# Performance work log

Hardware: AMD Instinct MI355X
Metric: run time of the kernel (lower is better)

## Reference

```python
import jax, jax.numpy as jnp
import numpy as np

N = 4096       # number of graph nodes
F_IN = 512     # in_features == out_features (residual connection requires it)
H = 8          # n_heads


def setup_inputs() -> dict:
    key = jax.random.key(0)
    k1, k2, k3, k4, k5 = jax.random.split(key, 5)
    s = 1.0 / np.sqrt(F_IN)  # keep projections well-scaled
    x = jax.random.normal(k1, (N, F_IN), dtype=jnp.float32)
    Wq = jax.random.normal(k2, (F_IN, F_IN), dtype=jnp.float32) * s
    Wk = jax.random.normal(k3, (F_IN, F_IN), dtype=jnp.float32) * s
    Wv = jax.random.normal(k4, (F_IN, F_IN), dtype=jnp.float32) * s
    adj = jax.random.randint(k5, (H, N, N), 0, 2, dtype=jnp.int32)
    return {"x": x, "Wq": Wq, "Wk": Wk, "Wv": Wv, "adj": adj}


def reference(x, Wq, Wk, Wv, adj):
    # Faithful to torch GraphAttentionLayer.forward (eval mode, dropout off).
    # NOTE: the torch code builds keys = input.repeat(N,1,1).detach() -> the
    # K/V inputs are stop-gradient copies of x; projections are per-node, so
    # we compute them once instead of materializing the redundant [N,N,F].
    n, f = x.shape
    d = f // H  # head dim (chunk_size)
    xk = jax.lax.stop_gradient(x)
    # nn.Linear: y = x @ W.T ; split feature dim into heads -> [H, N, d]
    Q = (x @ Wq.T).reshape(n, H, d).transpose(1, 0, 2)
    K = (xk @ Wk.T).reshape(n, H, d).transpose(1, 0, 2)
    V = (xk @ Wv.T).reshape(n, H, d).transpose(1, 0, 2)
    # scaled by sqrt(in_features) (NOT head dim), as in the original
    scores = jnp.einsum('hnd,hmd->hnm', Q, K) / jnp.sqrt(jnp.float32(f))
    scores = jnp.where(adj > 0, scores, jnp.float32(-9e15))
    attn = jax.nn.softmax(scores, axis=-1)          # [H, N, N]
    out = jnp.einsum('hnm,hmd->hnd', attn, V)       # [H, N, d]
    out = out.transpose(1, 0, 2).reshape(n, f)      # concat heads -> [N, F]
    return jax.nn.elu(out + x)[:, None, :]          # [N, 1, F] like torch
```

## Files before the change

### kernel.cpp

```cpp
#include <hip/hip_runtime.h>
#include <hip/hip_bf16.h>

#define NN 4096
#define FF 512
#define NH 8
#define DH 64

typedef __attribute__((ext_vector_type(8))) short bf16x8;
typedef __attribute__((ext_vector_type(4))) float f32x4;

#define X_OFF  0
#define W_OFF  2097152
#define QF_OFF 2883584
#define KF_OFF 4980736
#define VF_OFF 7077888
#define PACC_OFF 9175040
#define PDEN_USHORT_OFF 13369344

__device__ __forceinline__ ushort f2bf(float f) {
    __hip_bfloat16 h = __float2bfloat16(f);
    return __builtin_bit_cast(ushort, h);
}
__device__ __forceinline__ float bf2f(ushort u) {
    unsigned int v = ((unsigned int)u) << 16;
    return __builtin_bit_cast(float, v);
}

__global__ __launch_bounds__(256) void cvt_kernel(const float* __restrict__ x,
                                                  const float* __restrict__ wq,
                                                  const float* __restrict__ wk,
                                                  const float* __restrict__ wv,
                                                  ushort* __restrict__ ws) {
    int i = blockIdx.x * 256 + threadIdx.x;
    int base = i * 4;
    const float* src;
    int off;
    float sc = 1.f;
    if (base < 2097152) { src = x; off = base; }
    else {
        int t = base - 2097152;
        int m = t >> 18;
        src = (m == 0) ? wq : ((m == 1) ? wk : wv);
        if (m == 0) sc = 0.044194173824159216f;
        off = t & 262143;
    }
    float4 v = *reinterpret_cast<const float4*>(src + off);
    ushort4 o;
    o.x = f2bf(v.x * sc); o.y = f2bf(v.y * sc); o.z = f2bf(v.z * sc); o.w = f2bf(v.w * sc);
    *reinterpret_cast<ushort4*>(ws + base) = o;
}

__global__ __launch_bounds__(256) void qkv_kernel(ushort* __restrict__ ws) {
    int bx = blockIdx.x;
    int mat = bx >> 3;
    int fb  = bx & 7;
    int mb  = blockIdx.y;
    int wave = threadIdx.x >> 6, lane = threadIdx.x & 63;
    int la = lane & 15, lk = lane >> 4;

    int m_base = mb * 64 + wave * 16;
    int f_base = fb * 64;

    const ushort* xb = ws + X_OFF;
    const ushort* wb = ws + W_OFF + mat * 262144;

    f32x4 acc[4];
#pragma unroll
    for (int t = 0; t < 4; ++t) acc[t] = (f32x4){0.f, 0.f, 0.f, 0.f};

#pragma unroll 4
    for (int k0 = 0; k0 < 512; k0 += 32) {
        bf16x8 a = *reinterpret_cast<const bf16x8*>(xb + (size_t)(m_base + la) * 512 + k0 + lk * 8);
#pragma unroll
        for (int ft = 0; ft < 4; ++ft) {
            bf16x8 b = *reinterpret_cast<const bf16x8*>(wb + (size_t)(f_base + ft * 16 + la) * 512 + k0 + lk * 8);
            acc[ft] = __builtin_amdgcn_mfma_f32_16x16x32_bf16(a, b, acc[ft], 0, 0, 0);
        }
    }

#pragma unroll
    for (int ft = 0; ft < 4; ++ft) {
#pragma unroll
        for (int r = 0; r < 4; ++r) {
            int n = m_base + lk * 4 + r;
            int d = ft * 16 + la;
            ushort v = f2bf(acc[ft][r]);
            if (mat < 2) {
                ushort* base = ws + (mat == 0 ? QF_OFF : KF_OFF) + (size_t)fb * 262144;
                int blk = n >> 4, rr = n & 15;
                int half = d >> 5, lkk = (d >> 3) & 3, e = d & 7;
                base[(((size_t)blk * 2 + half) * 64 + lkk * 16 + rr) * 8 + e] = v;
            } else {
                ushort* base = ws + VF_OFF + (size_t)fb * 262144;
                int kb64 = n >> 6, kc = n & 63;
                int hf = kc >> 5, lkv = (kc >> 3) & 3, ev = kc & 7;
                int dt = d >> 4, lav = d & 15;
                base[((((size_t)kb64 * 4 + dt) * 2 + hf) * 64 + lkv * 16 + lav) * 8 + ev] = v;
            }
        }
    }
}


#define ATTN_BODY(ADJ_CUR, ADJ_NXT, KB, KBN)                                              \
    {                                                                                     \
        const int kb64_ = (KB);                                                           \
        bf16x8 kf[4][2], vb[4][2];                                                        \
        _Pragma("unroll")                                                                 \
        for (int kt = 0; kt < 4; ++kt) {                                                  \
            const ushort* kp = Kh + (((size_t)(kb64_ * 4 + kt) * 2) * 64 + lane) * 8;     \
            kf[kt][0] = *reinterpret_cast<const bf16x8*>(kp);                             \
            kf[kt][1] = *reinterpret_cast<const bf16x8*>(kp + 512);                       \
        }                                                                                 \
        _Pragma("unroll")                                                                 \
        for (int dt = 0; dt < 4; ++dt) {                                                  \
            const ushort* vp = Vh + ((((size_t)kb64_ * 4 + dt) * 2) * 64 + lane) * 8;     \
            vb[dt][0] = *reinterpret_cast<const bf16x8*>(vp);                             \
            vb[dt][1] = *reinterpret_cast<const bf16x8*>(vp + 512);                       \
        }                                                                                 \
        {         \
            int colb_ = (KBN) * 64 + la;                                                  \
            _Pragma("unroll")                                                             \
            for (int qs = 0; qs < 2; ++qs)                                                \
                _Pragma("unroll")                                                         \
                for (int r = 0; r < 4; ++r)                                               \
                    _Pragma("unroll")                                                     \
                    for (int kt = 0; kt < 4; ++kt)                                        \
                        ADJ_NXT[qs][r][kt] = __builtin_nontemporal_load(                  \
                            adjh + rowoff[qs][r] + colb_ + kt * 16);                      \
        }                                                                                 \
        f32x4 s[2][4];                                                                    \
        _Pragma("unroll")                                                                 \
        for (int kt = 0; kt < 4; ++kt)                                                    \
            _Pragma("unroll")                                                             \
            for (int qs = 0; qs < 2; ++qs) {                                              \
                s[qs][kt] = __builtin_amdgcn_mfma_f32_16x16x32_bf16(qa[qs][0], kf[kt][0], zero, 0, 0, 0); \
                s[qs][kt] = __builtin_amdgcn_mfma_f32_16x16x32_bf16(qa[qs][1], kf[kt][1], s[qs][kt], 0, 0, 0); \
            }                                                                             \
        _Pragma("unroll")                                                                 \
        for (int qs = 0; qs < 2; ++qs)                                                    \
            _Pragma("unroll")                                                             \
            for (int kt = 0; kt < 4; ++kt)                                                \
                _Pragma("unroll")                                                         \
                for (int r = 0; r < 4; ++r) {                                             \
                    float sv = ADJ_CUR[qs][r][kt] ? s[qs][kt][r] : -1e30f;                \
                    float e = __expf(sv);                                                 \
                    den[qs][r] += e;                                                      \
                    P[wave][qs * 16 + lk * 4 + r][kt * 16 + la] = f2bf(e);                \
                }                                                                         \
        _Pragma("unroll")                                                                 \
        for (int qs = 0; qs < 2; ++qs) {                                                  \
            bf16x8 pa0 = *reinterpret_cast<const bf16x8*>(&P[wave][qs * 16 + la][lk * 8]);      \
            bf16x8 pa1 = *reinterpret_cast<const bf16x8*>(&P[wave][qs * 16 + la][32 + lk * 8]); \
            _Pragma("unroll")                                                             \
            for (int dt = 0; dt < 4; ++dt) {                                              \
                acc[qs][dt] = __builtin_amdgcn_mfma_f32_16x16x32_bf16(pa0, vb[dt][0], acc[qs][dt], 0, 0, 0); \
                acc[qs][dt] = __builtin_amdgcn_mfma_f32_16x16x32_bf16(pa1, vb[dt][1], acc[qs][dt], 0, 0, 0); \
            }                                                                             \
        }                                                                                 \
    }

__global__ __launch_bounds__(256, 2) void attn_kernel(const int* __restrict__ adj,
                                                      const ushort* __restrict__ ws,
                                                      ushort* __restrict__ pacc,
                                                      float* __restrict__ pden) {
    __shared__ ushort P[4][32][72];

    int bid = blockIdx.x;
    int h = bid & 7, qb = (bid >> 3) & 31, ks = bid >> 8;
    int wave = threadIdx.x >> 6, lane = threadIdx.x & 63;
    int la = lane & 15, lk = lane >> 4;
    int q0 = qb * 128 + wave * 32;

    const ushort* Qh = ws + QF_OFF + (size_t)h * 262144;
    const ushort* Kh = ws + KF_OFF + (size_t)h * 262144;
    const ushort* Vh = ws + VF_OFF + (size_t)h * 262144;
    const int* adjh = adj + (size_t)h * 16777216;

    bf16x8 qa[2][2];
#pragma unroll
    for (int qs = 0; qs < 2; ++qs)
#pragma unroll
        for (int hf = 0; hf < 2; ++hf)
            qa[qs][hf] = *reinterpret_cast<const bf16x8*>(
                Qh + ((((size_t)((q0 >> 4) + qs)) * 2 + hf) * 64 + lane) * 8);

    f32x4 acc[2][4];
    float den[2][4];
    int rowoff[2][4];
#pragma unroll
    for (int qs = 0; qs < 2; ++qs)
#pragma unroll
        for (int r = 0; r < 4; ++r) {
            acc[qs][r] = (f32x4){0.f, 0.f, 0.f, 0.f};
            den[qs][r] = 0.f;
            rowoff[qs][r] = (q0 + qs * 16 + lk * 4 + r) * 4096;
        }

    const f32x4 zero = {0.f, 0.f, 0.f, 0.f};
    int kbase = ks * 32;

    int adjA[2][4][4], adjB[2][4][4];
    {
        int colb_ = kbase * 64 + la;
#pragma unroll
        for (int qs = 0; qs < 2; ++qs)
#pragma unroll
            for (int r = 0; r < 4; ++r)
#pragma unroll
                for (int kt = 0; kt < 4; ++kt)
                    adjA[qs][r][kt] = __builtin_nontemporal_load(
                        adjh + rowoff[qs][r] + colb_ + kt * 16);
    }

    for (int it = 0; it < 32; it += 2) {
        int k0 = kbase + it;
        int k2n = (it + 2 < 32) ? (k0 + 2) : kbase;
        ATTN_BODY(adjA, adjB, k0, k0 + 1)
        ATTN_BODY(adjB, adjA, k0 + 1, k2n)
    }

#pragma unroll
    for (int qs = 0; qs < 2; ++qs)
#pragma unroll
        for (int r = 0; r < 4; ++r)
#pragma unroll
            for (int m = 1; m < 16; m <<= 1)
                den[qs][r] += __shfl_xor(den[qs][r], m, 64);

    ushort* pa_out = pacc + ((size_t)ks * 8 + h) * 4096 * 64;
#pragma unroll
    for (int qs = 0; qs < 2; ++qs)
#pragma unroll
        for (int dt = 0; dt < 4; ++dt)
#pragma unroll
            for (int r = 0; r < 4; ++r) {
                int q = q0 + qs * 16 + lk * 4 + r;
                __builtin_nontemporal_store(f2bf(acc[qs][dt][r]), pa_out + (size_t)q * 64 + dt * 16 + la);
            }
    if (la == 0) {
        float* pd = pden + ((size_t)ks * 8 + h) * 4096;
#pragma unroll
        for (int qs = 0; qs < 2; ++qs)
#pragma unroll
            for (int r = 0; r < 4; ++r)
                pd[q0 + qs * 16 + lk * 4 + r] = den[qs][r];
    }
}

__global__ __launch_bounds__(256) void combine_kernel(const float* __restrict__ x,
                                                      const ushort* __restrict__ pacc,
                                                      const float* __restrict__ pden,
                                                      float* __restrict__ out) {
    int idx = blockIdx.x * 256 + threadIdx.x;
    int n = idx >> 7, fq = idx & 127;
    int h = fq >> 4;
    int d4 = (fq & 15) * 4;

    float4 o = make_float4(0.f, 0.f, 0.f, 0.f);
    float den = 0.f;
#pragma unroll
    for (int ksp = 0; ksp < 2; ++ksp) {
        const ushort* pa = pacc + (((size_t)ksp * 8 + h) * 4096 + n) * 64 + d4;
        ushort4 p = *reinterpret_cast<const ushort4*>(pa);
        o.x += bf2f(p.x); o.y += bf2f(p.y); o.z += bf2f(p.z); o.w += bf2f(p.w);
        den += pden[((size_t)ksp * 8 + h) * 4096 + n];
    }
    float4 xv = *reinterpret_cast<const float4*>(x + (size_t)n * 512 + fq * 4);
    float inv = 1.f / den;
    float4 r;
    r.x = o.x * inv + xv.x;
    r.y = o.y * inv + xv.y;
    r.z = o.z * inv + xv.z;
    r.w = o.w * inv + xv.w;
    r.x = (r.x > 0.f) ? r.x : (__expf(r.x) - 1.f);
    r.y = (r.y > 0.f) ? r.y : (__expf(r.y) - 1.f);
    r.z = (r.z > 0.f) ? r.z : (__expf(r.z) - 1.f);
    r.w = (r.w > 0.f) ? r.w : (__expf(r.w) - 1.f);
    *reinterpret_cast<float4*>(out + (size_t)n * 512 + fq * 4) = r;
}

extern "C" void kernel_launch(void* const* d_in, const int* in_sizes, int n_in,
                              void* d_out, int out_size, void* d_ws, size_t ws_size,
                              hipStream_t stream) {
    const float* x  = (const float*)d_in[0];
    const float* wq = (const float*)d_in[1];
    const float* wk = (const float*)d_in[2];
    const float* wv = (const float*)d_in[3];
    const int*   adj = (const int*)d_in[4];
    float* out = (float*)d_out;
    ushort* ws = (ushort*)d_ws;
    ushort* pacc = ws + PACC_OFF;
    float* pden = (float*)(ws + PDEN_USHORT_OFF);

    cvt_kernel<<<2816, 256, 0, stream>>>(x, wq, wk, wv, ws);
    qkv_kernel<<<dim3(24, 64), 256, 0, stream>>>(ws);
    attn_kernel<<<512, 256, 0, stream>>>(adj, ws, pacc, pden);
    combine_kernel<<<2048, 256, 0, stream>>>(x, pacc, pden, out);
}
```

Baseline: 234.2 us.

## Pre-pack int32 adjacency into bitmasks with a ballot kernel before attention

Measured after the change: 258.7 us. 1.1x slower.

```diff
diff --git a/kernel.cpp b/kernel.cpp
--- a/kernel.cpp
+++ b/kernel.cpp
@@ -16,6 +16,7 @@
 #define VF_OFF 7077888
 #define PACC_OFF 9175040
 #define PDEN_USHORT_OFF 13369344
+#define PK_USHORT_OFF 16777216
 
 __device__ __forceinline__ ushort f2bf(float f) {
     __hip_bfloat16 h = __float2bfloat16(f);
@@ -24,6 +25,30 @@
 __device__ __forceinline__ float bf2f(ushort u) {
     unsigned int v = ((unsigned int)u) << 16;
     return __builtin_bit_cast(float, v);
+}
+
+__global__ __launch_bounds__(256) void pack_kernel(const int* __restrict__ adj,
+                                                   unsigned int* __restrict__ pk) {
+    int wave = threadIdx.x >> 6, lane = threadIdx.x & 63;
+    int row = blockIdx.x * 4 + wave;
+    const int* ar = adj + (size_t)row * 4096;
+    unsigned long long* outp = reinterpret_cast<unsigned long long*>(pk + (size_t)row * 128);
+    for (int it = 0; it < 64; it += 4) {
+        int v0 = __builtin_nontemporal_load(ar + (it + 0) * 64 + lane);
+        int v1 = __builtin_nontemporal_load(ar + (it + 1) * 64 + lane);
+        int v2 = __builtin_nontemporal_load(ar + (it + 2) * 64 + lane);
+        int v3 = __builtin_nontemporal_load(ar + (it + 3) * 64 + lane);
+        unsigned long long b0 = __ballot(v0 != 0);
+        unsigned long long b1 = __ballot(v1 != 0);
+        unsigned long long b2 = __ballot(v2 != 0);
+        unsigned long long b3 = __ballot(v3 != 0);
+        if (lane == 0) {
+            outp[it + 0] = b0;
+            outp[it + 1] = b1;
+            outp[it + 2] = b2;
+            outp[it + 3] = b3;
+        }
+    }
 }
 
 __global__ __launch_bounds__(256) void cvt_kernel(const float* __restrict__ x,
@@ -102,7 +127,7 @@
 }
 
 
-#define ATTN_BODY(ADJ_CUR, ADJ_NXT, KB, KBN)                                              \
+#define ATTN_BODY(M_CUR, M_NXT, KB, KBN)                                                  \
     {                                                                                     \
         const int kb64_ = (KB);                                                           \
         bf16x8 kf[4][2], vb[4][2];                                                        \
@@ -118,17 +143,11 @@
             vb[dt][0] = *reinterpret_cast<const bf16x8*>(vp);                             \
             vb[dt][1] = *reinterpret_cast<const bf16x8*>(vp + 512);                       \
         }                                                                                 \
-        {         \
-            int colb_ = (KBN) * 64 + la;                                                  \
+        _Pragma("unroll")                                                                 \
+        for (int qs = 0; qs < 2; ++qs)                                                    \
             _Pragma("unroll")                                                             \
-            for (int qs = 0; qs < 2; ++qs)                                                \
-                _Pragma("unroll")                                                         \
-                for (int r = 0; r < 4; ++r)                                               \
-                    _Pragma("unroll")                                                     \
-                    for (int kt = 0; kt < 4; ++kt)                                        \
-                        ADJ_NXT[qs][r][kt] = __builtin_nontemporal_load(                  \
-                            adjh + rowoff[qs][r] + colb_ + kt * 16);                      \
-        }                                                                                 \
+            for (int r = 0; r < 4; ++r)                                                   \
+                M_NXT[qs][r] = *reinterpret_cast<const uint2*>(pkh + rowpk[qs][r] + (KBN) * 2); \
         f32x4 s[2][4];                                                                    \
         _Pragma("unroll")                                                                 \
         for (int kt = 0; kt < 4; ++kt)                                                    \
@@ -140,14 +159,16 @@
         _Pragma("unroll")                                                                 \
         for (int qs = 0; qs < 2; ++qs)                                                    \
             _Pragma("unroll")                                                             \
-            for (int kt = 0; kt < 4; ++kt)                                                \
+            for (int kt = 0; kt < 4; ++kt) {                                              \
                 _Pragma("unroll")                                                         \
                 for (int r = 0; r < 4; ++r) {                                             \
-                    float sv = ADJ_CUR[qs][r][kt] ? s[qs][kt][r] : -1e30f;                \
+                    unsigned int dw = (kt < 2) ? M_CUR[qs][r].x : M_CUR[qs][r].y;         \
+                    float sv = ((dw >> (la + ((kt & 1) << 4))) & 1u) ? s[qs][kt][r] : -1e30f; \
                     float e = __expf(sv);                                                 \
                     den[qs][r] += e;                                                      \
                     P[wave][qs * 16 + lk * 4 + r][kt * 16 + la] = f2bf(e);                \
                 }                                                                         \
+            }                                                                             \
         _Pragma("unroll")                                                                 \
         for (int qs = 0; qs < 2; ++qs) {                                                  \
             bf16x8 pa0 = *reinterpret_cast<const bf16x8*>(&P[wave][qs * 16 + la][lk * 8]);      \
@@ -160,7 +181,7 @@
         }                                                                                 \
     }
 
-__global__ __launch_bounds__(256, 2) void attn_kernel(const int* __restrict__ adj,
+__global__ __launch_bounds__(256, 2) void attn_kernel(const unsigned int* __restrict__ pk,
                                                       const ushort* __restrict__ ws,
                                                       ushort* __restrict__ pacc,
                                                       float* __restrict__ pden) {
@@ -175,7 +196,7 @@
     const ushort* Qh = ws + QF_OFF + (size_t)h * 262144;
     const ushort* Kh = ws + KF_OFF + (size_t)h * 262144;
     const ushort* Vh = ws + VF_OFF + (size_t)h * 262144;
-    const int* adjh = adj + (size_t)h * 16777216;
+    const unsigned int* pkh = pk + (size_t)h * 4096 * 128;
 
     bf16x8 qa[2][2];
 #pragma unroll
@@ -187,37 +208,33 @@
 
     f32x4 acc[2][4];
     float den[2][4];
-    int rowoff[2][4];
+    int rowpk[2][4];
 #pragma unroll
     for (int qs = 0; qs < 2; ++qs)
 #pragma unroll
         for (int r = 0; r < 4; ++r) {
             acc[qs][r] = (f32x4){0.f, 0.f, 0.f, 0.f};
             den[qs][r] = 0.f;
-            rowoff[qs][r] = (q0 + qs * 16 + lk * 4 + r) * 4096;
+            rowpk[qs][r] = (q0 + qs * 16 + lk * 4 + r) * 128;
         }
 
     const f32x4 zero = {0.f, 0.f, 0.f, 0.f};
     int kbase = ks * 32;
 
-    int adjA[2][4][4], adjB[2][4][4];
+    uint2 mA[2][4], mB[2][4];
     {
-        int colb_ = kbase * 64 + la;
 #pragma unroll
         for (int qs = 0; qs < 2; ++qs)
 #pragma unroll
             for (int r = 0; r < 4; ++r)
-#pragma unroll
-                for (int kt = 0; kt < 4; ++kt)
-                    adjA[qs][r][kt] = __builtin_nontemporal_load(
-                        adjh + rowoff[qs][r] + colb_ + kt * 16);
+                mA[qs][r] = *reinterpret_cast<const uint2*>(pkh + rowpk[qs][r] + kbase * 2);
     }
 
     for (int it = 0; it < 32; it += 2) {
         int k0 = kbase + it;
         int k2n = (it + 2 < 32) ? (k0 + 2) : kbase;
-        ATTN_BODY(adjA, adjB, k0, k0 + 1)
-        ATTN_BODY(adjB, adjA, k0 + 1, k2n)
+        ATTN_BODY(mA, mB, k0, k0 + 1)
+        ATTN_BODY(mB, mA, k0 + 1, k2n)
     }
 
 #pragma unroll
@@ -292,9 +309,11 @@
     ushort* ws = (ushort*)d_ws;
     ushort* pacc = ws + PACC_OFF;
     float* pden = (float*)(ws + PDEN_USHORT_OFF);
-
+    unsigned int* pk = (unsigned int*)(ws + PK_USHORT_OFF);
+
+    pack_kernel<<<8192, 256, 0, stream>>>(adj, pk);
     cvt_kernel<<<2816, 256, 0, stream>>>(x, wq, wk, wv, ws);
     qkv_kernel<<<dim3(24, 64), 256, 0, stream>>>(ws);
-    attn_kernel<<<512, 256, 0, stream>>>(adj, ws, pacc, pden);
+    attn_kernel<<<512, 256, 0, stream>>>(pk, ws, pacc, pden);
     combine_kernel<<<2048, 256, 0, stream>>>(x, pacc, pden, out);
 }
```
